# Kernel tuning notes

Measured on AMD Instinct MI355X. Metric: run time of the kernel, lower is better.

The kernel has to match this reference:

```python
import jax, jax.numpy as jnp
import numpy as np
from jax import lax

BETA = 0.3

def setup_inputs() -> dict:
    key = jax.random.key(0)
    ks = jax.random.split(key, 5)
    B, C, H, W = 1, 64, 96, 96
    x = jax.random.normal(ks[0], (B, C, H, W), dtype=jnp.float32)
    # d_conv: Conv2d(C, C, k=3, stride=1, padding=2, dilation=2)
    dW = jax.random.normal(ks[1], (C, C, 3, 3), dtype=jnp.float32) * 0.05
    db = jax.random.normal(ks[2], (C,), dtype=jnp.float32) * 0.05
    # conv: Conv2d(C, C, k=1)
    cW = jax.random.normal(ks[3], (C, C, 1, 1), dtype=jnp.float32) * 0.1
    cb = jax.random.normal(ks[4], (C,), dtype=jnp.float32) * 0.05
    return {"x": x, "dW": dW, "db": db, "cW": cW, "cb": cb}

def _conv(x, w, b, padding, dilation):
    y = lax.conv_general_dilated(
        x, w, window_strides=(1, 1),
        padding=[(padding, padding), (padding, padding)],
        rhs_dilation=(dilation, dilation),
        dimension_numbers=("NCHW", "OIHW", "NCHW"))
    return y + b[None, :, None, None]

def reference(x, dW, db, cW, cb):
    B, C, H, W = x.shape
    HW = H * W
    y = _conv(x, dW, db, padding=2, dilation=2)   # (B,C,H,W), same d_conv used for q and k
    v = _conv(x, cW, cb, padding=0, dilation=1).reshape(B, HW, C)
    # NOTE: torch uses raw .reshape (not transpose) for q — faithful here.
    q = y.reshape(B, HW, C)
    k = y.reshape(B, C, HW)
    qk = jnp.einsum("bnc,bcm->bnm", q, k)         # (B,HW,HW)
    qk = jnp.where(jnp.abs(qk) > BETA, qk, 0.0)   # threshold mask (qk*mask)
    att = jax.nn.softmax(qk, axis=-1)
    att = jnp.einsum("bnm,bmc->bnc", att, v)      # (B,HW,C)
    att = att.swapaxes(1, 2).reshape(B, C, H, W)
    return x + att
```

## Files before the change

kernel.cpp:

```cpp
#include <hip/hip_runtime.h>
#include <hip/hip_bf16.h>

#define CC 64
#define HW 9216
#define IMG 96
#define SPLITS 16
#define SPLEN 576
#define ITERS 9
#define LOG2E 1.44269504f
#define RESC 5.545f

typedef _Float16 f16;
typedef __attribute__((ext_vector_type(8))) _Float16 f16x8;
typedef __attribute__((ext_vector_type(4))) _Float16 f16x4;
typedef __attribute__((ext_vector_type(4))) float f32x4;
typedef __attribute__((ext_vector_type(16))) float f32x16;
typedef __attribute__((ext_vector_type(4))) unsigned int u32x4;

__global__ __launch_bounds__(256) void prepad_kernel(
    const float* __restrict__ x, const float* __restrict__ dW, const float* __restrict__ cW,
    f16* __restrict__ xt, f16* __restrict__ dWt, f16* __restrict__ cWt)
{
    __shared__ float tile[32][65];
    const int t = threadIdx.x;
    if (blockIdx.x >= 313) {
        const int wb = blockIdx.x - 313;
        #pragma unroll
        for (int j = 0; j < 4; ++j) {
            int idx = wb * 1024 + j * 256 + t;
            if (idx < 36864) {
                float val = dW[idx];
                int co = idx / 576;
                int r = idx - co * 576;
                int ci = r / 9, tap = r - ci * 9;
                dWt[tap * 4096 + co * 64 + ci] = (f16)val;
            } else {
                int c = idx - 36864;
                cWt[c] = (f16)cW[c];
            }
        }
        return;
    }
    const int p0 = blockIdx.x * 32;
    const int pl = t & 31;
    const int p = p0 + pl;
    int r = p / 100, c = p % 100;
    bool interior = (r >= 2) && (r < 98) && (c >= 2) && (c < 98);
    int img = (r - 2) * IMG + (c - 2);
    #pragma unroll
    for (int j = 0; j < 8; ++j) {
        int ci = j * 8 + (t >> 5);
        tile[pl][ci] = interior ? x[ci * HW + img] : 0.f;
    }
    __syncthreads();
    const int row16 = t >> 4, chunk = t & 15;
    #pragma unroll
    for (int j = 0; j < 2; ++j) {
        int row = j * 16 + row16;
        int pr = p0 + row;
        if (pr < 10000) {
            f16x4 hv = {(f16)tile[row][chunk * 4 + 0], (f16)tile[row][chunk * 4 + 1],
                        (f16)tile[row][chunk * 4 + 2], (f16)tile[row][chunk * 4 + 3]};
            *(f16x4*)&xt[pr * 64 + chunk * 4] = hv;
        }
    }
}

__global__ __launch_bounds__(64) void conv_mfma_kernel(
    const f16* __restrict__ xt, const f16* __restrict__ dWt, const float* __restrict__ db,
    const f16* __restrict__ cWt, const float* __restrict__ cb,
    f16* __restrict__ yq, f16* __restrict__ kt, f16* __restrict__ vt)
{
    const int b = blockIdx.x;
    const int tile = b >> 2, cog = b & 3;
    const int co0 = cog * 16;
    const int L = threadIdx.x;
    const int g = L >> 4, c16 = L & 15;

    f16x8 Bf[9][2], Bv[2];
    #pragma unroll
    for (int tap = 0; tap < 9; ++tap)
        #pragma unroll
        for (int kc = 0; kc < 2; ++kc)
            Bf[tap][kc] = *(const f16x8*)&dWt[(tap * 64 + co0 + c16) * 64 + g * 8 + kc * 32];
    #pragma unroll
    for (int kc = 0; kc < 2; ++kc)
        Bv[kc] = *(const f16x8*)&cWt[(co0 + c16) * 64 + g * 8 + kc * 32];

    const int ms = tile * 16;
    const int h = ms / IMG, wc = ms % IMG;
    const int pb = (h + 2) * 100 + (wc + 2) + c16;

    f32x4 accY = (f32x4){0.f, 0.f, 0.f, 0.f};
    f32x4 accV = (f32x4){0.f, 0.f, 0.f, 0.f};

    #pragma unroll
    for (int tap = 0; tap < 9; ++tap) {
        int kh = tap / 3, kw = tap % 3;
        int toff = (2 * kh - 2) * 100 + (2 * kw - 2);
        const f16* ap = xt + (pb + toff) * 64;
        f16x8 A0 = *(const f16x8*)(ap + g * 8);
        f16x8 A1 = *(const f16x8*)(ap + g * 8 + 32);
        accY = __builtin_amdgcn_mfma_f32_16x16x32_f16(A0, Bf[tap][0], accY, 0, 0, 0);
        accY = __builtin_amdgcn_mfma_f32_16x16x32_f16(A1, Bf[tap][1], accY, 0, 0, 0);
        if (tap == 4) {
            accV = __builtin_amdgcn_mfma_f32_16x16x32_f16(A0, Bv[0], accV, 0, 0, 0);
            accV = __builtin_amdgcn_mfma_f32_16x16x32_f16(A1, Bv[1], accV, 0, 0, 0);
        }
    }

    const float dbv = db[co0 + c16], cbv = cb[co0 + c16];
    f16 hy[4];
    #pragma unroll
    for (int j = 0; j < 4; ++j) hy[j] = (f16)(accY[j] + dbv);
    *(f16x4*)&yq[(co0 + c16) * HW + ms + 4 * g] = (f16x4){hy[0], hy[1], hy[2], hy[3]};
    #pragma unroll
    for (int j = 0; j < 4; ++j)
        kt[(ms + 4 * g + j) * 64 + co0 + c16] = hy[j];
    #pragma unroll
    for (int j = 0; j < 4; ++j) {
        int m = ms + 4 * g + j;
        vt[(m & 63) * HW + (co0 + c16) * 144 + (m >> 6)] = (f16)(accV[j] + cbv);
    }
}

__global__ __launch_bounds__(256, 4) void attn_kernel(
    const f16* __restrict__ kt, const f16* __restrict__ vt, const f16* __restrict__ yq,
    f16* __restrict__ acc_ws, float* __restrict__ m_ws, float* __restrict__ l_ws)
{
    __shared__ f16 sKT[64 * 64];
    __shared__ f16 sVT[64 * 64];
    __shared__ float sAL[4 * 32];

    const int t = threadIdx.x;
    const int L = t & 63, w = t >> 6;
    const int l5 = L >> 5, l31 = L & 31;
    const int x7 = l31 & 7;
    const int qb = blockIdx.x >> 4, sp = blockIdx.x & (SPLITS - 1);
    const int n0 = qb * 128;
    const int mbase = sp * SPLEN;
    float* alw = (float*)sAL + w * 32;

    const int srow0 = t >> 3, sch = t & 7;
    const int srow1 = srow0 + 32;
    const int dst0 = srow0 * 64 + ((sch ^ (srow0 & 7)) << 3);
    const int dst1 = srow1 * 64 + ((sch ^ (srow1 & 7)) << 3);

    f16x8 qf[4];
    #pragma unroll
    for (int kc = 0; kc < 4; ++kc)
        qf[kc] = *(const f16x8*)(yq + (n0 + w * 32 + l31) * 64 + kc * 16 + l5 * 8);

    float mi = -1e30f, mtrue = -1e30f, li = 0.f;
    f32x16 acc[2];
    #pragma unroll
    for (int ct = 0; ct < 2; ++ct)
        #pragma unroll
        for (int r = 0; r < 16; ++r) acc[ct][r] = 0.f;

    for (int it = 0; it < ITERS; ++it) {
        const int m0 = mbase + it * 64;
        uint4 rK0 = *(const uint4*)&kt[(m0 + srow0) * 64 + sch * 8];
        uint4 rK1 = *(const uint4*)&kt[(m0 + srow1) * 64 + sch * 8];
        uint4 rV0 = *(const uint4*)&vt[srow0 * HW + m0 + sch * 8];
        uint4 rV1 = *(const uint4*)&vt[srow1 * HW + m0 + sch * 8];
        __syncthreads();
        *(uint4*)&sKT[dst0] = rK0;
        *(uint4*)&sKT[dst1] = rK1;
        *(uint4*)&sVT[dst0] = rV0;
        *(uint4*)&sVT[dst1] = rV1;
        __syncthreads();

        f32x16 st[2];
        #pragma unroll
        for (int kt2 = 0; kt2 < 2; ++kt2) {
            f32x16 d;
            #pragma unroll
            for (int r = 0; r < 16; ++r) d[r] = 0.f;
            #pragma unroll
            for (int kc = 0; kc < 4; ++kc) {
                f16x8 af = *(const f16x8*)&sKT[(kt2 * 32 + l31) * 64 + ((((kc << 1) | l5) ^ x7) << 3)];
                d = __builtin_amdgcn_mfma_f32_32x32x16_f16(af, qf[kc], d, 0, 0, 0);
            }
            st[kt2] = d;
        }
        #pragma unroll
        for (int kt2 = 0; kt2 < 2; ++kt2)
            #pragma unroll
            for (int r = 0; r < 16; ++r)
                st[kt2][r] = (fabsf(st[kt2][r]) > 0.3f) ? st[kt2][r] : 0.f;

        float q8[8];
        #pragma unroll
        for (int kt2 = 0; kt2 < 2; ++kt2)
            #pragma unroll
            for (int rq = 0; rq < 4; ++rq)
                q8[kt2 * 4 + rq] = fmaxf(fmaxf(st[kt2][rq * 4 + 0], st[kt2][rq * 4 + 1]),
                                         fmaxf(st[kt2][rq * 4 + 2], st[kt2][rq * 4 + 3]));
        float mx = fmaxf(fmaxf(fmaxf(q8[0], q8[1]), fmaxf(q8[2], q8[3])),
                         fmaxf(fmaxf(q8[4], q8[5]), fmaxf(q8[6], q8[7])));
        mx = fmaxf(mx, __shfl_xor(mx, 32, 64));
        mtrue = fmaxf(mtrue, mx);

        unsigned long long need = __ballot(mx > mi + RESC);
        if (need) {
            float mnew = fmaxf(mi, mx);
            float alpha = __builtin_amdgcn_exp2f((mi - mnew) * LOG2E);
            li *= alpha;
            if (l5 == 0) alw[l31] = alpha;
            f32x4 aj[4];
            #pragma unroll
            for (int rq = 0; rq < 4; ++rq)
                aj[rq] = *(const f32x4*)&alw[rq * 8 + l5 * 4];
            #pragma unroll
            for (int ct = 0; ct < 2; ++ct)
                #pragma unroll
                for (int r = 0; r < 16; ++r)
                    acc[ct][r] *= aj[r >> 2][r & 3];
            mi = mnew;
        }
        const float nL = mi * LOG2E;

        float ls = 0.f;
        unsigned int u[2][4][2];
        #pragma unroll
        for (int kt2 = 0; kt2 < 2; ++kt2)
            #pragma unroll
            for (int rq = 0; rq < 4; ++rq) {
                float p0 = __builtin_amdgcn_exp2f(fmaf(st[kt2][rq * 4 + 0], LOG2E, -nL));
                float p1 = __builtin_amdgcn_exp2f(fmaf(st[kt2][rq * 4 + 1], LOG2E, -nL));
                float p2 = __builtin_amdgcn_exp2f(fmaf(st[kt2][rq * 4 + 2], LOG2E, -nL));
                float p3 = __builtin_amdgcn_exp2f(fmaf(st[kt2][rq * 4 + 3], LOG2E, -nL));
                ls += (p0 + p1) + (p2 + p3);
                u[kt2][rq][0] = __builtin_bit_cast(unsigned int, __builtin_amdgcn_cvt_pkrtz(p0, p1));
                u[kt2][rq][1] = __builtin_bit_cast(unsigned int, __builtin_amdgcn_cvt_pkrtz(p2, p3));
            }
        li += ls;

        #pragma unroll
        for (int kc = 0; kc < 4; ++kc) {
            const int kt2 = kc >> 1;
            const int rq0 = (kc & 1) * 2, rq1 = rq0 + 1;
            auto rA = __builtin_amdgcn_permlane32_swap(
                (int)u[kt2][rq0][0], (int)u[kt2][rq1][0], false, false);
            auto rB = __builtin_amdgcn_permlane32_swap(
                (int)u[kt2][rq0][1], (int)u[kt2][rq1][1], false, false);
            u32x4 pw = {(unsigned int)rA[0], (unsigned int)rB[0],
                        (unsigned int)rA[1], (unsigned int)rB[1]};
            f16x8 pa = __builtin_bit_cast(f16x8, pw);
            #pragma unroll
            for (int ct = 0; ct < 2; ++ct) {
                int vrow = ct * 32 + l31;
                f16x8 vb = *(const f16x8*)&sVT[vrow * 64 + ((((kc << 1) | l5) ^ x7) << 3)];
                acc[ct] = __builtin_amdgcn_mfma_f32_32x32x16_f16(pa, vb, acc[ct], 0, 0, 0);
            }
        }
    }

    float fsc = __builtin_amdgcn_exp2f((mi - mtrue) * LOG2E);
    li *= fsc;
    float li_tot = li + __shfl_xor(li, 32, 64);
    if (l5 == 0) alw[l31] = fsc;
    f32x4 fj[4];
    #pragma unroll
    for (int rq = 0; rq < 4; ++rq)
        fj[rq] = *(const f32x4*)&alw[rq * 8 + l5 * 4];
    #pragma unroll
    for (int ct = 0; ct < 2; ++ct)
        #pragma unroll
        for (int r = 0; r < 16; ++r)
            acc[ct][r] *= fj[r >> 2][r & 3];

    const int base = blockIdx.x;
    #pragma unroll
    for (int ct = 0; ct < 2; ++ct)
        #pragma unroll
        for (int r = 0; r < 16; ++r) {
            int ql = w * 32 + (r & 3) + 8 * (r >> 2) + 4 * l5;
            int c  = ct * 32 + l31;
            acc_ws[base * 8192 + ql * 64 + c] = (f16)acc[ct][r];
        }
    if (l5 == 0) {
        m_ws[base * 128 + w * 32 + l31] = mtrue;
        l_ws[base * 128 + w * 32 + l31] = li_tot;
    }
}

__global__ __launch_bounds__(256) void merge_kernel(
    const f16* __restrict__ acc_ws, const float* __restrict__ m_ws, const float* __restrict__ l_ws,
    const float* __restrict__ x, float* __restrict__ out)
{
    __shared__ float wsh[SPLITS * 16];
    __shared__ float att[64 * 17];
    const int b = blockIdx.x;
    const int row0 = b * 16;
    const int qb = row0 >> 7;
    const int ql0 = row0 & 127;
    const int t = threadIdx.x;
    if (t < 16) {
        int ql = ql0 + t;
        float ms = -1e30f;
        float mv[SPLITS];
        #pragma unroll
        for (int sp = 0; sp < SPLITS; ++sp) {
            mv[sp] = m_ws[(qb * SPLITS + sp) * 128 + ql];
            ms = fmaxf(ms, mv[sp]);
        }
        float Lsum = 0.f, ev[SPLITS];
        #pragma unroll
        for (int sp = 0; sp < SPLITS; ++sp) {
            ev[sp] = __builtin_amdgcn_exp2f((mv[sp] - ms) * LOG2E);
            Lsum += l_ws[(qb * SPLITS + sp) * 128 + ql] * ev[sp];
        }
        float inv = 1.f / Lsum;
        #pragma unroll
        for (int sp = 0; sp < SPLITS; ++sp)
            wsh[sp * 16 + t] = ev[sp] * inv;
    }
    __syncthreads();
    for (int i = t; i < 1024; i += 256) {
        int rr = i >> 6, c = i & 63;
        float v = 0.f;
        #pragma unroll
        for (int sp = 0; sp < SPLITS; ++sp)
            v += (float)acc_ws[(qb * SPLITS + sp) * 8192 + (ql0 + rr) * 64 + c] * wsh[sp * 16 + rr];
        att[c * 17 + rr] = v;
    }
    __syncthreads();
    for (int i = t; i < 1024; i += 256) {
        int c = i >> 4, r = i & 15;
        int idx = c * HW + row0 + r;
        out[idx] = x[idx] + att[c * 17 + r];
    }
}

extern "C" void kernel_launch(void* const* d_in, const int* in_sizes, int n_in,
                              void* d_out, int out_size, void* d_ws, size_t ws_size,
                              hipStream_t stream)
{
    const float* x  = (const float*)d_in[0];
    const float* dW = (const float*)d_in[1];
    const float* db = (const float*)d_in[2];
    const float* cW = (const float*)d_in[3];
    const float* cb = (const float*)d_in[4];
    float* out = (float*)d_out;

    char* ws = (char*)d_ws;
    f16* kt     = (f16*)(ws);
    f16* yq     = (f16*)(ws + 1179648);
    f16* vt     = (f16*)(ws + 2359296);
    f16* xt     = (f16*)(ws + 3538944);
    f16* dWt    = (f16*)(ws + 4818944);
    f16* cWt    = (f16*)(ws + 4892672);
    f16* acc_ws = (f16*)(ws + 4900864);
    float* m_ws = (float*)(ws + 23775232);
    float* l_ws = (float*)(ws + 24365056);

    prepad_kernel<<<dim3(353), dim3(256), 0, stream>>>(x, dW, cW, xt, dWt, cWt);
    conv_mfma_kernel<<<dim3(2304), dim3(64), 0, stream>>>(xt, dWt, db, cWt, cb, yq, kt, vt);
    attn_kernel<<<dim3(72 * SPLITS), dim3(256), 0, stream>>>(kt, vt, yq, acc_ws, m_ws, l_ws);
    merge_kernel<<<dim3(576), dim3(256), 0, stream>>>(acc_ws, m_ws, l_ws, x, out);
}
```

Measured before the change: 136.2 us.

## Double-buffer K/V tiles in attention loop using async global-to-LDS loads

```diff
diff --git a/kernel.cpp b/kernel.cpp
--- a/kernel.cpp
+++ b/kernel.cpp
@@ -16,6 +16,10 @@
 typedef __attribute__((ext_vector_type(4))) float f32x4;
 typedef __attribute__((ext_vector_type(16))) float f32x16;
 typedef __attribute__((ext_vector_type(4))) unsigned int u32x4;
+
+#define GLOAD(gp, lp) __builtin_amdgcn_global_load_lds(                      \
+    (const __attribute__((address_space(1))) void*)(gp),                     \
+    (__attribute__((address_space(3))) void*)(lp), 16, 0, 0)
 
 __global__ __launch_bounds__(256) void prepad_kernel(
     const float* __restrict__ x, const float* __restrict__ dW, const float* __restrict__ cW,
@@ -128,8 +132,8 @@
     const f16* __restrict__ kt, const f16* __restrict__ vt, const f16* __restrict__ yq,
     f16* __restrict__ acc_ws, float* __restrict__ m_ws, float* __restrict__ l_ws)
 {
-    __shared__ f16 sKT[64 * 64];
-    __shared__ f16 sVT[64 * 64];
+    __shared__ f16 sKT[2][64 * 64];
+    __shared__ f16 sVT[2][64 * 64];
     __shared__ float sAL[4 * 32];
 
     const int t = threadIdx.x;
@@ -141,10 +145,9 @@
     const int mbase = sp * SPLEN;
     float* alw = (float*)sAL + w * 32;
 
-    const int srow0 = t >> 3, sch = t & 7;
-    const int srow1 = srow0 + 32;
-    const int dst0 = srow0 * 64 + ((sch ^ (srow0 & 7)) << 3);
-    const int dst1 = srow1 * 64 + ((sch ^ (srow1 & 7)) << 3);
+    const int g3 = L >> 3;
+    const int gs = (L & 7) ^ g3;
+    const int rb = w * 16;
 
     f16x8 qf[4];
     #pragma unroll
@@ -158,18 +161,23 @@
         #pragma unroll
         for (int r = 0; r < 16; ++r) acc[ct][r] = 0.f;
 
+    GLOAD(kt + (mbase + rb + g3) * 64 + gs * 8,     &sKT[0][rb * 64]);
+    GLOAD(kt + (mbase + rb + 8 + g3) * 64 + gs * 8, &sKT[0][(rb + 8) * 64]);
+    GLOAD(vt + (rb + g3) * HW + mbase + gs * 8,     &sVT[0][rb * 64]);
+    GLOAD(vt + (rb + 8 + g3) * HW + mbase + gs * 8, &sVT[0][(rb + 8) * 64]);
+
     for (int it = 0; it < ITERS; ++it) {
-        const int m0 = mbase + it * 64;
-        uint4 rK0 = *(const uint4*)&kt[(m0 + srow0) * 64 + sch * 8];
-        uint4 rK1 = *(const uint4*)&kt[(m0 + srow1) * 64 + sch * 8];
-        uint4 rV0 = *(const uint4*)&vt[srow0 * HW + m0 + sch * 8];
-        uint4 rV1 = *(const uint4*)&vt[srow1 * HW + m0 + sch * 8];
+        const int cur = it & 1;
         __syncthreads();
-        *(uint4*)&sKT[dst0] = rK0;
-        *(uint4*)&sKT[dst1] = rK1;
-        *(uint4*)&sVT[dst0] = rV0;
-        *(uint4*)&sVT[dst1] = rV1;
-        __syncthreads();
+
+        if (it + 1 < ITERS) {
+            const int m1 = mbase + (it + 1) * 64;
+            const int nx = cur ^ 1;
+            GLOAD(kt + (m1 + rb + g3) * 64 + gs * 8,     &sKT[nx][rb * 64]);
+            GLOAD(kt + (m1 + rb + 8 + g3) * 64 + gs * 8, &sKT[nx][(rb + 8) * 64]);
+            GLOAD(vt + (rb + g3) * HW + m1 + gs * 8,     &sVT[nx][rb * 64]);
+            GLOAD(vt + (rb + 8 + g3) * HW + m1 + gs * 8, &sVT[nx][(rb + 8) * 64]);
+        }
 
         f32x16 st[2];
         #pragma unroll
@@ -179,7 +187,7 @@
             for (int r = 0; r < 16; ++r) d[r] = 0.f;
             #pragma unroll
             for (int kc = 0; kc < 4; ++kc) {
-                f16x8 af = *(const f16x8*)&sKT[(kt2 * 32 + l31) * 64 + ((((kc << 1) | l5) ^ x7) << 3)];
+                f16x8 af = *(const f16x8*)&sKT[cur][(kt2 * 32 + l31) * 64 + ((((kc << 1) | l5) ^ x7) << 3)];
                 d = __builtin_amdgcn_mfma_f32_32x32x16_f16(af, qf[kc], d, 0, 0, 0);
             }
             st[kt2] = d;
@@ -251,7 +259,7 @@
             #pragma unroll
             for (int ct = 0; ct < 2; ++ct) {
                 int vrow = ct * 32 + l31;
-                f16x8 vb = *(const f16x8*)&sVT[vrow * 64 + ((((kc << 1) | l5) ^ x7) << 3)];
+                f16x8 vb = *(const f16x8*)&sVT[cur][vrow * 64 + ((((kc << 1) | l5) ^ x7) << 3)];
                 acc[ct] = __builtin_amdgcn_mfma_f32_32x32x16_f16(pa, vb, acc[ct], 0, 0, 0);
             }
         }
```

New measurement: 137.6 us. Within noise of the previous version (+1.0%).
